# Performance work log

Measured on AMD Instinct MI355X. Metric: run time of the kernel, lower is better.

## Reference

```python
import jax, jax.numpy as jnp
import numpy as np

# Fixed architecture constants from the source
B, T, D, V, L, H = 4096, 128, 64, 65, 3, 8
HD = D // H  # head_size = 8
DF = 4 * D   # 256


def _layernorm(x, g, b, eps=1e-5):
    mu = jnp.mean(x, axis=-1, keepdims=True)
    var = jnp.mean(jnp.square(x - mu), axis=-1, keepdims=True)
    return (x - mu) * jax.lax.rsqrt(var + eps) * g + b


def setup_inputs() -> dict:
    key = jax.random.key(0)
    ks = iter(jax.random.split(key, 64))
    s = 0.02
    n = lambda shape: jax.random.normal(next(ks), shape, dtype=jnp.float32) * s
    inp = {
        "tok_emb": n((V, D)),
        "pos_emb": n((T, D)),
        # per-block params stacked on leading layer dim L=3
        "ln1_g": jnp.ones((L, D), jnp.float32), "ln1_b": jnp.zeros((L, D), jnp.float32),
        "wq": n((L, D, D)), "wk": n((L, D, D)), "wv": n((L, D, D)),
        "wo": n((L, D, D)), "bo": jnp.zeros((L, D), jnp.float32),
        "ln2_g": jnp.ones((L, D), jnp.float32), "ln2_b": jnp.zeros((L, D), jnp.float32),
        "w1": n((L, D, DF)), "b1": jnp.zeros((L, DF), jnp.float32),
        "w2": n((L, DF, D)), "b2": jnp.zeros((L, D), jnp.float32),
        "lnf_g": jnp.ones((D,), jnp.float32), "lnf_b": jnp.zeros((D,), jnp.float32),
        "lm_w": n((D, V)), "lm_b": jnp.zeros((V,), jnp.float32),
        "idx": jax.random.randint(next(ks), (B, T), 0, V),
        "targets": jax.random.randint(next(ks), (B, T), 0, V),
    }
    return inp


def _forward(tok_emb, pos_emb, ln1_g, ln1_b, wq, wk, wv, wo, bo,
             ln2_g, ln2_b, w1, b1, w2, b2, lnf_g, lnf_b, lm_w, lm_b,
             idx, targets):
    b, t = idx.shape
    x = tok_emb[idx] + pos_emb[:t]  # [B,T,D]
    mask = jnp.tril(jnp.ones((t, t), bool))
    scale = 1.0 / np.sqrt(HD)
    for l in range(L):  # 3 structurally identical blocks (dropout = identity at eval)
        xn = _layernorm(x, ln1_g[l], ln1_b[l])
        # 8 per-head projections fused into one [D,D] matmul (concat along out dim)
        q = (xn @ wq[l]).reshape(b, t, H, HD)
        k = (xn @ wk[l]).reshape(b, t, H, HD)
        v = (xn @ wv[l]).reshape(b, t, H, HD)
        scores = jnp.einsum('bqhd,bkhd->bhqk', q, k) * scale
        scores = jnp.where(mask, scores, -jnp.inf)
        probs = jax.nn.softmax(scores, axis=-1)
        attn = jnp.einsum('bhqk,bkhd->bqhd', probs, v).reshape(b, t, D)
        x = x + attn @ wo[l] + bo[l]
        xn = _layernorm(x, ln2_g[l], ln2_b[l])
        x = x + jax.nn.relu(xn @ w1[l] + b1[l]) @ w2[l] + b2[l]
    x = _layernorm(x, lnf_g, lnf_b)
    logits = (x @ lm_w + lm_b).reshape(b * t, V)
    logp = jax.nn.log_softmax(logits, axis=-1)
    loss = -jnp.mean(jnp.take_along_axis(logp, targets.reshape(b * t, 1), axis=1))
    return logits, loss


def reference(tok_emb, pos_emb, ln1_g, ln1_b, wq, wk, wv, wo, bo,
              ln2_g, ln2_b, w1, b1, w2, b2, lnf_g, lnf_b, lm_w, lm_b,
              idx, targets):
    return _forward(tok_emb, pos_emb, ln1_g, ln1_b, wq, wk, wv, wo, bo,
                    ln2_g, ln2_b, w1, b1, w2, b2, lnf_g, lnf_b, lm_w, lm_b,
                    idx, targets)
```

## Files before the change

### kernel.cpp

```cpp
#include <hip/hip_runtime.h>
#include <hip/hip_bf16.h>

#define NB  4096
#define NT  128
#define ND  64
#define NV  65
#define NL  3
#define NH  8
#define NDF 256
#define NBT (NB*NT)

#define OFF_TOK   0
#define OFF_POS   4160
#define OFF_LN1G  12352
#define OFF_LN1B  12544
#define OFF_WQ    12736
#define OFF_WK    25024
#define OFF_WV    37312
#define OFF_WO    49600
#define OFF_BO    61888
#define OFF_LN2G  62080
#define OFF_LN2B  62272
#define OFF_W1    62464
#define OFF_B1    111616
#define OFF_W2    112384
#define OFF_B2    161536
#define OFF_LNFG  161728
#define OFF_LNFB  161792
#define OFF_LMW   161856
#define OFF_LMB   166016
#define CVT_TOTAL 166081
#define OFF_LOSS  166144
#define OFF_FLAG  166145

#define PKF       166148
#define PK_ELEMS  147456
#define NEED_WS   ((size_t)(PKF + PK_ELEMS) * 4)

typedef short s8v  __attribute__((ext_vector_type(8)));
typedef float f4v  __attribute__((ext_vector_type(4)));

struct CvtArgs { const void* p[19]; };

__device__ __forceinline__ unsigned short f2bf(float x) {
    unsigned int u = __float_as_uint(x);
    u = (u + 0x7fffu + ((u >> 16) & 1u)) >> 16;
    return (unsigned short)u;
}
__device__ __forceinline__ float bf2f(unsigned short h) {
    return __uint_as_float(((unsigned int)h) << 16);
}
__device__ __forceinline__ f4v mfma16(s8v a, s8v b, f4v c) {
    return __builtin_amdgcn_mfma_f32_16x16x32_bf16(a, b, c, 0, 0, 0);
}

__global__ void diag_fill(float* __restrict__ out, int n, float val) {
    int i = blockIdx.x * 256 + threadIdx.x;
    if (i < n) out[i] = val;
}

__global__ void detect_float(const unsigned short* __restrict__ tok,
                             int* __restrict__ flags) {
    int bad = 0;
    for (int i = threadIdx.x; i < 4096; i += 256) {
        float v = __uint_as_float(((unsigned int)tok[i]) << 16);
        if (!(fabsf(v) < 1000.f)) bad = 1;
    }
    if (bad) atomicOr(flags, 1);
}

__global__ void detect_int(const int* __restrict__ idx32,
                           int* __restrict__ flags) {
    int proven = 0;
    #pragma unroll
    for (int j = 0; j < 8; j++) {
        int slot = 2 * (threadIdx.x * 8 + j) + 1;
        if (idx32[slot] != 0) proven = 1;
    }
    if (proven) atomicOr(flags, 4);
}

__global__ void cvt_params(CvtArgs a, float* __restrict__ W,
                           const int* __restrict__ flags) {
    int tid = blockIdx.x * 256 + threadIdx.x;
    if (tid >= CVT_TOTAL) return;
    const int offs[20] = {0,4160,12352,12544,12736,25024,37312,49600,61888,
                          62080,62272,62464,111616,112384,161536,161728,
                          161792,161856,166016,166081};
    int s = 0;
    #pragma unroll
    for (int k = 1; k < 19; k++) s += (tid >= offs[k]);
    int local = tid - offs[s];
    if (*flags & 1) {
        W[tid] = ((const float*)a.p[s])[local];
    } else {
        unsigned int v = ((const unsigned short*)a.p[s])[local];
        W[tid] = __uint_as_float(v << 16);
    }
}

__global__ void pack_weights(const float* __restrict__ W,
                             unsigned short* __restrict__ pkw) {
    int p = blockIdx.x * 256 + threadIdx.x;
    if (p >= PK_ELEMS) return;
    int srcoff, K, N, perlay, local, ktbits;
    if (p < 49152) {
        int grp = p / 12288; local = p % 12288;
        srcoff = (grp == 0) ? OFF_WQ : (grp == 1) ? OFF_WK
               : (grp == 2) ? OFF_WV : OFF_WO;
        K = 64; N = 64; perlay = 4096; ktbits = 1;
    } else if (p < 98304) {
        local = p - 49152; srcoff = OFF_W1; K = 64; N = 256;
        perlay = 16384; ktbits = 1;
    } else {
        local = p - 98304; srcoff = OFF_W2; K = 256; N = 64;
        perlay = 16384; ktbits = 3;
    }
    int lay = local / perlay, rem = local % perlay;
    int t = rem >> 9, le = rem & 511, l = le >> 3, e = le & 7;
    int kt = t & ((1 << ktbits) - 1), nt = t >> ktbits;
    int row = kt * 32 + (l >> 4) * 8 + e;
    int col = nt * 16 + (l & 15);
    float v = W[srcoff + lay * K * N + row * N + col];
    unsigned short hi = f2bf(v);
    pkw[p] = hi;
    pkw[PK_ELEMS + p] = f2bf(v - bf2f(hi));
}

__global__ void mfma_probe(int* __restrict__ flags) {
    int l = threadIdx.x;
    s8v av, bv;
    int i = l & 15;
    #pragma unroll
    for (int e = 0; e < 8; e++) {
        int k = (l >> 4) * 8 + e;
        av[e] = (short)f2bf((float)(((i * 5 + k * 3) & 7) - 3));
        bv[e] = (short)f2bf((float)(((k * 7 + i * 11) & 7) - 4));
    }
    f4v c = {0.f, 0.f, 0.f, 0.f};
    c = mfma16(av, bv, c);
    int bad = 0;
    #pragma unroll
    for (int reg = 0; reg < 4; reg++) {
        int row = (l >> 4) * 4 + reg, col = l & 15;
        float exp = 0.f;
        for (int k = 0; k < 32; k++)
            exp += (float)(((row * 5 + k * 3) & 7) - 3) *
                   (float)(((k * 7 + col * 11) & 7) - 4);
        if (c[reg] != exp) bad = 1;
    }
    if (bad) atomicOr(flags, 8);
}

__device__ __forceinline__ void unpack8(uint4 u, float* f) {
    f[0] = __uint_as_float(u.x << 16); f[1] = __uint_as_float(u.x & 0xffff0000u);
    f[2] = __uint_as_float(u.y << 16); f[3] = __uint_as_float(u.y & 0xffff0000u);
    f[4] = __uint_as_float(u.z << 16); f[5] = __uint_as_float(u.z & 0xffff0000u);
    f[6] = __uint_as_float(u.w << 16); f[7] = __uint_as_float(u.w & 0xffff0000u);
}

__device__ __forceinline__ void ln_rm(const float (*src)[68], float (*dst)[68],
                                      const float* __restrict__ g,
                                      const float* __restrict__ bb, int tid) {
    int r = tid >> 3, q = tid & 7;
    int c0 = q * 8;
    float s = 0.f, s2 = 0.f;
    #pragma unroll
    for (int c = 0; c < 8; c++) { float v = src[r][c0 + c]; s += v; s2 += v * v; }
    s += __shfl_xor(s, 1);  s2 += __shfl_xor(s2, 1);
    s += __shfl_xor(s, 2);  s2 += __shfl_xor(s2, 2);
    s += __shfl_xor(s, 4);  s2 += __shfl_xor(s2, 4);
    float mu   = s  * (1.f / 64.f);
    float var  = s2 * (1.f / 64.f) - mu * mu;
    float rstd = rsqrtf(var + 1e-5f);
    #pragma unroll
    for (int c = 0; c < 8; c++) {
        int cc = c0 + c;
        dst[r][cc] = (src[r][cc] - mu) * rstd * g[cc] + bb[cc];
    }
}

__device__ __forceinline__ void ln_frag(const float (*src)[68],
        unsigned short* __restrict__ dhi, unsigned short* __restrict__ dlo,
        const float* __restrict__ g, const float* __restrict__ bb, int tid) {
    int r = tid >> 3, q = tid & 7, c0 = q * 8;
    float s = 0.f, s2 = 0.f;
    #pragma unroll
    for (int c = 0; c < 8; c++) { float v = src[r][c0 + c]; s += v; s2 += v * v; }
    s += __shfl_xor(s, 1);  s2 += __shfl_xor(s2, 1);
    s += __shfl_xor(s, 2);  s2 += __shfl_xor(s2, 2);
    s += __shfl_xor(s, 4);  s2 += __shfl_xor(s2, 4);
    float mu   = s  * (1.f / 64.f);
    float var  = s2 * (1.f / 64.f) - mu * mu;
    float rstd = rsqrtf(var + 1e-5f);
    unsigned uh[4], ul[4];
    #pragma unroll
    for (int c2 = 0; c2 < 4; c2++) {
        float y0 = (src[r][c0 + c2*2    ] - mu) * rstd * g[c0 + c2*2    ] + bb[c0 + c2*2    ];
        float y1 = (src[r][c0 + c2*2 + 1] - mu) * rstd * g[c0 + c2*2 + 1] + bb[c0 + c2*2 + 1];
        unsigned short h0 = f2bf(y0), h1 = f2bf(y1);
        uh[c2] = (unsigned)h0 | ((unsigned)h1 << 16);
        ul[c2] = (unsigned)f2bf(y0 - bf2f(h0)) | ((unsigned)f2bf(y1 - bf2f(h1)) << 16);
    }
    int di = (((r >> 4) * 2 + (q >> 2)) * 64 + (q & 3) * 16 + (r & 15)) * 8;
    *(uint4*)(dhi + di) = make_uint4(uh[0], uh[1], uh[2], uh[3]);
    *(uint4*)(dlo + di) = make_uint4(ul[0], ul[1], ul[2], ul[3]);
}

__device__ __forceinline__ void fma16(const float* xr, const float* wr, float& a) {
    float4 x0 = *(const float4*)(xr);
    float4 x1 = *(const float4*)(xr + 4);
    float4 x2 = *(const float4*)(xr + 8);
    float4 x3 = *(const float4*)(xr + 12);
    a = fmaf(x0.x, wr[0],  a); a = fmaf(x0.y, wr[1],  a);
    a = fmaf(x0.z, wr[2],  a); a = fmaf(x0.w, wr[3],  a);
    a = fmaf(x1.x, wr[4],  a); a = fmaf(x1.y, wr[5],  a);
    a = fmaf(x1.z, wr[6],  a); a = fmaf(x1.w, wr[7],  a);
    a = fmaf(x2.x, wr[8],  a); a = fmaf(x2.y, wr[9],  a);
    a = fmaf(x2.z, wr[10], a); a = fmaf(x2.w, wr[11], a);
    a = fmaf(x3.x, wr[12], a); a = fmaf(x3.y, wr[13], a);
    a = fmaf(x3.z, wr[14], a); a = fmaf(x3.w, wr[15], a);
}

__device__ void ln_scalar(const float* x, float* o,
                          const float* g, const float* bb) {
    float mu = 0.f;
    for (int i = 0; i < ND; i++) mu += x[i];
    mu *= (1.f / 64.f);
    float var = 0.f;
    for (int i = 0; i < ND; i++) { float d = x[i] - mu; var += d * d; }
    var *= (1.f / 64.f);
    float rstd = rsqrtf(var + 1e-5f);
    for (int i = 0; i < ND; i++) o[i] = (x[i] - mu) * rstd * g[i] + bb[i];
}

__global__ __launch_bounds__(1024, 4) void gpt_fwd(
    const float* __restrict__ W, const unsigned short* __restrict__ pkw,
    int usepk, const void* __restrict__ idxp, const void* __restrict__ tgtp,
    float* __restrict__ out, float* __restrict__ loss_acc,
    const int* __restrict__ flags)
{
    __shared__ alignas(16) float xs[NT][68];
    __shared__ alignas(16) unsigned char regB[34816];
    __shared__ alignas(16) unsigned char uni[65536];
    __shared__ alignas(16) unsigned short zblk[8];
    __shared__ float wsum[16];

    float (*xnR)[68] = (float (*)[68])regB;
    unsigned short* xah = (unsigned short*)regB;
    unsigned short* xal = (unsigned short*)(regB + 16384);
    unsigned short* q_lds = (unsigned short*)uni;
    unsigned short* k_lds = (unsigned short*)(uni + 16384);
    unsigned short* vb    = (unsigned short*)(uni + 32768);
    unsigned short (*qs)[72] = (unsigned short (*)[72])(uni);
    unsigned short (*ks)[72] = (unsigned short (*)[72])(uni + 18432);
    unsigned short (*vs)[72] = (unsigned short (*)[72])(uni + 36864);
    unsigned short* ha = (unsigned short*)uni;
    unsigned short* hl = (unsigned short*)(uni + 32768);
    float (*hch)[264] = (float (*)[264])uni;

    const int tid  = threadIdx.x;
    const int lane = tid & 63;
    const int w    = tid >> 6;
    const int b    = blockIdx.x;
    const int fl   = *flags;
    const bool i64 = !(fl & 4);
    const bool use_mfma = usepk && !(fl & 8);
    const int*       idx32 = (const int*)idxp;
    const long long* idx64 = (const long long*)idxp;
    const int*       tgt32 = (const int*)tgtp;
    const long long* tgt64 = (const long long*)tgtp;

    if (tid < 8) zblk[tid] = 0;

    for (int e = tid * 4; e < NT * ND; e += 4096) {
        int r = e >> 6, c = e & 63;
        int n = b * NT + r;
        int tok = i64 ? (int)idx64[n] : idx32[n];
        float4 te = *(const float4*)&W[OFF_TOK + tok * ND + c];
        float4 pe = *(const float4*)&W[OFF_POS + r * ND + c];
        float4 xv;
        xv.x = te.x + pe.x; xv.y = te.y + pe.y;
        xv.z = te.z + pe.z; xv.w = te.w + pe.w;
        *(float4*)&xs[r][c] = xv;
    }
    __syncthreads();

    if (use_mfma) {
        for (int lay = 0; lay < NL; lay++) {
            ln_frag(xs, xah, xal, W + OFF_LN1G + lay * 64, W + OFF_LN1B + lay * 64, tid);
            __syncthreads();

            {
                const unsigned short* pbase = pkw + lay * 4096;
                #pragma unroll 1
                for (int i = 0; i < 6; i++) {
                    int ft = w * 6 + i;
                    int mat = ft >> 5, mt = (ft >> 2) & 7, nt = ft & 3;
                    const unsigned short* pb = pbase + mat * 12288 + nt * 1024 + lane * 8;
                    f4v acc = {0.f, 0.f, 0.f, 0.f};
                    #pragma unroll
                    for (int kt = 0; kt < 2; kt++) {
                        s8v ah = *(const s8v*)(xah + ((mt * 2 + kt) * 64 + lane) * 8);
                        s8v al = *(const s8v*)(xal + ((mt * 2 + kt) * 64 + lane) * 8);
                        s8v bh = *(const s8v*)(pb + kt * 512);
                        s8v bl = *(const s8v*)(pb + PK_ELEMS + kt * 512);
                        acc = mfma16(ah, bh, acc);
                        acc = mfma16(ah, bl, acc);
                        acc = mfma16(al, bh, acc);
                    }
                    int row0 = mt * 16 + (lane >> 4) * 4;
                    int fullcol = nt * 16 + (lane & 15);
                    int head = fullcol >> 3, dim = fullcol & 7;
                    if (mat == 0) {
                        #pragma unroll
                        for (int i2 = 0; i2 < 4; i2++)
                            q_lds[(head * 128 + row0 + i2) * 8 + dim] =
                                f2bf(acc[i2] * 0.35355339059327373f);
                    } else if (mat == 1) {
                        #pragma unroll
                        for (int i2 = 0; i2 < 4; i2++)
                            k_lds[(head * 128 + row0 + i2) * 8 + dim] = f2bf(acc[i2]);
                    } else {
                        #pragma unroll
                        for (int i2 = 0; i2 < 4; i2++) {
                            int key = row0 + i2;
                            vb[((((head * 4) + (key >> 5)) * 4 + ((key >> 3) & 3)) * 8
                                + dim) * 8 + (key & 7)] = f2bf(acc[i2]);
                        }
                    }
                }
            }
            __syncthreads();

            {
                unsigned short* pscr = (unsigned short*)(uni + 49152) + w * 512;
                const int cl = lane & 15, g = lane >> 4;
                #pragma unroll 1
                for (int ti = 0; ti < 4; ti++) {
                    int t = w + ti * 16;
                    int mt = t >> 3, head = t & 7;
                    const unsigned short* qsrc = (lane < 16)
                        ? q_lds + (head * 128 + mt * 16 + cl) * 8 : zblk;
                    s8v qa = *(const s8v*)qsrc;
                    f4v sv[8];
                    #pragma unroll
                    for (int nt = 0; nt < 8; nt++) {
                        sv[nt] = (f4v){0.f, 0.f, 0.f, 0.f};
                        if (nt <= mt) {
                            const unsigned short* ksrc = (lane < 16)
                                ? k_lds + (head * 128 + nt * 16 + cl) * 8 : zblk;
                            s8v kb = *(const s8v*)ksrc;
                            sv[nt] = mfma16(qa, kb, sv[nt]);
                            if (nt == mt) {
                                #pragma unroll
                                for (int i2 = 0; i2 < 4; i2++)
                                    sv[nt][i2] = (cl <= g * 4 + i2) ? sv[nt][i2] : -1e30f;
                            }
                        }
                    }
                    float mx[4] = {-1e30f, -1e30f, -1e30f, -1e30f};
                    #pragma unroll
                    for (int nt = 0; nt < 8; nt++)
                        if (nt <= mt) {
                            #pragma unroll
                            for (int i2 = 0; i2 < 4; i2++)
                                mx[i2] = fmaxf(mx[i2], sv[nt][i2]);
                        }
                    #pragma unroll
                    for (int i2 = 0; i2 < 4; i2++) {
                        mx[i2] = fmaxf(mx[i2], __shfl_xor(mx[i2], 1));
                        mx[i2] = fmaxf(mx[i2], __shfl_xor(mx[i2], 2));
                        mx[i2] = fmaxf(mx[i2], __shfl_xor(mx[i2], 4));
                        mx[i2] = fmaxf(mx[i2], __shfl_xor(mx[i2], 8));
                    }
                    float sm[4] = {0.f, 0.f, 0.f, 0.f};
                    #pragma unroll
                    for (int nt = 0; nt < 8; nt++)
                        if (nt <= mt) {
                            #pragma unroll
                            for (int i2 = 0; i2 < 4; i2++) {
                                float p = __expf(sv[nt][i2] - mx[i2]);
                                sv[nt][i2] = p;
                                sm[i2] += p;
                            }
                        }
                    #pragma unroll
                    for (int i2 = 0; i2 < 4; i2++) {
                        sm[i2] += __shfl_xor(sm[i2], 1);
                        sm[i2] += __shfl_xor(sm[i2], 2);
                        sm[i2] += __shfl_xor(sm[i2], 4);
                        sm[i2] += __shfl_xor(sm[i2], 8);
                    }
                    float inv[4];
                    #pragma unroll
                    for (int i2 = 0; i2 < 4; i2++) inv[i2] = 1.f / sm[i2];
                    f4v o = {0.f, 0.f, 0.f, 0.f};
                    #pragma unroll
                    for (int kt = 0; kt < 4; kt++) {
                        if (kt <= (mt >> 1)) {
                            #pragma unroll
                            for (int s2 = 0; s2 < 2; s2++) {
                                int nt = kt * 2 + s2;
                                #pragma unroll
                                for (int i2 = 0; i2 < 4; i2++) {
                                    float pv = (nt <= mt) ? sv[nt][i2] * inv[i2] : 0.f;
                                    pscr[(g * 4 + i2) * 32 + s2 * 16 + cl] = f2bf(pv);
                                }
                            }
                            s8v pa = *(const s8v*)(pscr + cl * 32 + g * 8);
                            const unsigned short* vsrc = (cl < 8)
                                ? vb + ((((head * 4) + kt) * 4 + g) * 8 + cl) * 8 : zblk;
                            s8v vf = *(const s8v*)vsrc;
                            o = mfma16(pa, vf, o);
                        }
                    }
                    if (cl < 8) {
                        #pragma unroll
                        for (int i2 = 0; i2 < 4; i2++) {
                            int r = mt * 16 + g * 4 + i2;
                            float y = o[i2];
                            unsigned short h = f2bf(y);
                            int di = (((r >> 4) * 2 + (head >> 2)) * 64
                                      + (head & 3) * 16 + (r & 15)) * 8 + cl;
                            xah[di] = h;
                            xal[di] = f2bf(y - bf2f(h));
                        }
                    }
                }
            }
            __syncthreads();

            {
                const unsigned short* pbase = pkw + 36864 + lay * 4096;
                const float* bo = W + OFF_BO + lay * 64;
                #pragma unroll 1
                for (int i = 0; i < 2; i++) {
                    int ft = w * 2 + i;
                    int mt = ft >> 2, nt = ft & 3;
                    const unsigned short* pb = pbase + nt * 1024 + lane * 8;
                    f4v acc = {0.f, 0.f, 0.f, 0.f};
                    #pragma unroll
                    for (int kt = 0; kt < 2; kt++) {
                        s8v ah = *(const s8v*)(xah + ((mt * 2 + kt) * 64 + lane) * 8);
                        s8v al = *(const s8v*)(xal + ((mt * 2 + kt) * 64 + lane) * 8);
                        s8v bh = *(const s8v*)(pb + kt * 512);
                        s8v bl = *(const s8v*)(pb + PK_ELEMS + kt * 512);
                        acc = mfma16(ah, bh, acc);
                        acc = mfma16(ah, bl, acc);
                        acc = mfma16(al, bh, acc);
                    }
                    int row0 = mt * 16 + (lane >> 4) * 4, col = nt * 16 + (lane & 15);
                    float bias = bo[col];
                    xs[row0    ][col] += acc[0] + bias;
                    xs[row0 + 1][col] += acc[1] + bias;
                    xs[row0 + 2][col] += acc[2] + bias;
                    xs[row0 + 3][col] += acc[3] + bias;
                }
            }
            __syncthreads();

            ln_frag(xs, xah, xal, W + OFF_LN2G + lay * 64, W + OFF_LN2B + lay * 64, tid);
            __syncthreads();

            for (int hh = 0; hh < 2; hh++) {
                {
                    const float* b1 = W + OFF_B1 + lay * 256;
                    #pragma unroll 1
                    for (int i = 0; i < 4; i++) {
                        int ft = w * 4 + i;
                        int mtl = ft >> 4, nt = ft & 15;
                        int mt = hh * 4 + mtl;
                        const unsigned short* pb = pkw + 49152 + lay * 16384 + nt * 1024 + lane * 8;
                        f4v acc = {0.f, 0.f, 0.f, 0.f};
                        #pragma unroll
                        for (int kt = 0; kt < 2; kt++) {
                            s8v ah = *(const s8v*)(xah + ((mt * 2 + kt) * 64 + lane) * 8);
                            s8v al = *(const s8v*)(xal + ((mt * 2 + kt) * 64 + lane) * 8);
                            s8v bh = *(const s8v*)(pb + kt * 512);
                            s8v bl = *(const s8v*)(pb + PK_ELEMS + kt * 512);
                            acc = mfma16(ah, bh, acc);
                            acc = mfma16(ah, bl, acc);
                            acc = mfma16(al, bh, acc);
                        }
                        int col = nt * 16 + (lane & 15);
                        float bias = b1[col];
                        int kt2 = col >> 5, q2 = (col >> 3) & 3, e2 = col & 7;
                        #pragma unroll
                        for (int i2 = 0; i2 < 4; i2++) {
                            int lr = mtl * 16 + (lane >> 4) * 4 + i2;
                            float hvv = fmaxf(acc[i2] + bias, 0.f);
                            int di = ((mtl * 8 + kt2) * 64 + q2 * 16 + (lr & 15)) * 8 + e2;
                            unsigned short hi = f2bf(hvv);
                            ha[di] = hi;
                            hl[di] = f2bf(hvv - bf2f(hi));
                        }
                    }
                }
                __syncthreads();
                {
                    const float* b2 = W + OFF_B2 + lay * 64;
                    int mtl = w >> 2, nt = w & 3;
                    const unsigned short* pb = pkw + 98304 + lay * 16384 + nt * 4096 + lane * 8;
                    f4v acc = {0.f, 0.f, 0.f, 0.f};
                    #pragma unroll 2
                    for (int kt = 0; kt < 8; kt++) {
                        s8v ah = *(const s8v*)(ha + ((mtl * 8 + kt) * 64 + lane) * 8);
                        s8v al = *(const s8v*)(hl + ((mtl * 8 + kt) * 64 + lane) * 8);
                        s8v bh = *(const s8v*)(pb + kt * 512);
                        s8v bl = *(const s8v*)(pb + PK_ELEMS + kt * 512);
                        acc = mfma16(ah, bh, acc);
                        acc = mfma16(ah, bl, acc);
                        acc = mfma16(al, bh, acc);
                    }
                    int row0 = hh * 64 + mtl * 16 + (lane >> 4) * 4, col = nt * 16 + (lane & 15);
                    float bias = b2[col];
                    xs[row0    ][col] += acc[0] + bias;
                    xs[row0 + 1][col] += acc[1] + bias;
                    xs[row0 + 2][col] += acc[2] + bias;
                    xs[row0 + 3][col] += acc[3] + bias;
                }
                __syncthreads();
            }
        }
        ln_rm(xs, xnR, W + OFF_LNFG, W + OFF_LNFB, tid);
        __syncthreads();
    } else {
        for (int lay = 0; lay < NL; lay++) {
            ln_rm(xs, xnR, W + OFF_LN1G + lay * 64, W + OFF_LN1B + lay * 64, tid);
            __syncthreads();
            {
                #pragma unroll 1
                for (int mmat = 0; mmat < 3; mmat++) {
                    const float* wm = W + (mmat == 0 ? OFF_WQ : (mmat == 1 ? OFF_WK : OFF_WV))
                                        + lay * ND * ND;
                    unsigned short (*dstp)[72] = (mmat == 0) ? qs : ((mmat == 1) ? ks : vs);
                    float acc[8];
                    #pragma unroll
                    for (int rr = 0; rr < 8; rr++) acc[rr] = 0.f;
                    #pragma unroll 1
                    for (int ih = 0; ih < 4; ih++) {
                        float wr[16];
                        #pragma unroll
                        for (int i = 0; i < 16; i++) wr[i] = wm[(ih * 16 + i) * ND + lane];
                        #pragma unroll
                        for (int rr = 0; rr < 8; rr++)
                            fma16(&xnR[w * 8 + rr][ih * 16], wr, acc[rr]);
                    }
                    #pragma unroll
                    for (int rr = 0; rr < 8; rr++)
                        dstp[w * 8 + rr][lane] = f2bf(acc[rr]);
                }
            }
            __syncthreads();
            {
                const int head = w & 7, hh = w >> 3;
                const int h8 = head * 8;
                const int r  = lane + hh * 64;
                const float scale = 0.35355339059327373f;
                float qv[8];
                uint4 qq = *(const uint4*)&qs[r][h8];
                unpack8(qq, qv);
                #pragma unroll
                for (int d = 0; d < 8; d++) qv[d] *= scale;
                float m = -1e30f, lsum = 0.f;
                float o[8] = {0, 0, 0, 0, 0, 0, 0, 0};
                for (int base = 0; base <= r; base += 8) {
                    float sc[8];
                    #pragma unroll
                    for (int t = 0; t < 8; t++) {
                        int kk = base + t; kk = kk > 127 ? 127 : kk;
                        uint4 kr = *(const uint4*)&ks[kk][h8];
                        float kf[8]; unpack8(kr, kf);
                        float s = 0.f;
                        #pragma unroll
                        for (int d = 0; d < 8; d++) s = fmaf(qv[d], kf[d], s);
                        sc[t] = (base + t <= r) ? s : -1e30f;
                    }
                    float cm = fmaxf(fmaxf(fmaxf(sc[0], sc[1]), fmaxf(sc[2], sc[3])),
                                     fmaxf(fmaxf(sc[4], sc[5]), fmaxf(sc[6], sc[7])));
                    float nm  = fmaxf(m, cm);
                    float fac = __expf(m - nm);
                    lsum *= fac;
                    #pragma unroll
                    for (int d = 0; d < 8; d++) o[d] *= fac;
                    #pragma unroll
                    for (int t = 0; t < 8; t++) {
                        float p = __expf(sc[t] - nm);
                        int kk = base + t; kk = kk > 127 ? 127 : kk;
                        uint4 vr = *(const uint4*)&vs[kk][h8];
                        float vf[8]; unpack8(vr, vf);
                        lsum += p;
                        #pragma unroll
                        for (int d = 0; d < 8; d++) o[d] = fmaf(p, vf[d], o[d]);
                    }
                    m = nm;
                }
                float inv = 1.f / lsum;
                #pragma unroll
                for (int d = 0; d < 8; d++) xnR[r][h8 + d] = o[d] * inv;
            }
            __syncthreads();
            {
                const float* wo = W + OFF_WO + lay * ND * ND;
                float acc[8];
                #pragma unroll
                for (int rr = 0; rr < 8; rr++) acc[rr] = W[OFF_BO + lay * ND + lane];
                #pragma unroll 1
                for (int ih = 0; ih < 4; ih++) {
                    float wr[16];
                    #pragma unroll
                    for (int i = 0; i < 16; i++) wr[i] = wo[(ih * 16 + i) * ND + lane];
                    #pragma unroll
                    for (int rr = 0; rr < 8; rr++)
                        fma16(&xnR[w * 8 + rr][ih * 16], wr, acc[rr]);
                }
                #pragma unroll
                for (int rr = 0; rr < 8; rr++)
                    xs[w * 8 + rr][lane] += acc[rr];
            }
            __syncthreads();
            ln_rm(xs, xnR, W + OFF_LN2G + lay * 64, W + OFF_LN2B + lay * 64, tid);
            __syncthreads();
            {
                const float* w1 = W + OFF_W1 + lay * ND * NDF;
                const float* w2 = W + OFF_W2 + lay * NDF * ND;
                const float* b1 = W + OFF_B1 + lay * NDF;
                const float* b2 = W + OFF_B2 + lay * ND;
                for (int ch = 0; ch < 4; ch++) {
                    int rbase = ch * 32;
                    {
                        int lr = tid >> 5;
                        int j0 = (tid & 31) * 8;
                        int r  = rbase + lr;
                        float4 ba  = *(const float4*)(b1 + j0);
                        float4 bb4 = *(const float4*)(b1 + j0 + 4);
                        float a0 = ba.x,  a1 = ba.y,  a2 = ba.z,  a3 = ba.w;
                        float a4 = bb4.x, a5 = bb4.y, a6 = bb4.z, a7 = bb4.w;
                        #pragma unroll 4
                        for (int i4 = 0; i4 < ND; i4 += 4) {
                            float4 xv = *(const float4*)&xnR[r][i4];
                            #pragma unroll
                            for (int s = 0; s < 4; s++) {
                                float xvs = (s == 0) ? xv.x : (s == 1) ? xv.y
                                          : (s == 2) ? xv.z : xv.w;
                                float4 wa = *(const float4*)(w1 + (i4 + s) * NDF + j0);
                                float4 wb = *(const float4*)(w1 + (i4 + s) * NDF + j0 + 4);
                                a0 = fmaf(xvs, wa.x, a0); a1 = fmaf(xvs, wa.y, a1);
                                a2 = fmaf(xvs, wa.z, a2); a3 = fmaf(xvs, wa.w, a3);
                                a4 = fmaf(xvs, wb.x, a4); a5 = fmaf(xvs, wb.y, a5);
                                a6 = fmaf(xvs, wb.z, a6); a7 = fmaf(xvs, wb.w, a7);
                            }
                        }
                        float4 h0, h1;
                        h0.x = fmaxf(a0, 0.f); h0.y = fmaxf(a1, 0.f);
                        h0.z = fmaxf(a2, 0.f); h0.w = fmaxf(a3, 0.f);
                        h1.x = fmaxf(a4, 0.f); h1.y = fmaxf(a5, 0.f);
                        h1.z = fmaxf(a6, 0.f); h1.w = fmaxf(a7, 0.f);
                        *(float4*)&hch[lr][j0]     = h0;
                        *(float4*)&hch[lr][j0 + 4] = h1;
                    }
                    __syncthreads();
                    {
                        int lr = tid >> 5;
                        int i0 = (tid & 31) * 2;
                        int r  = rbase + lr;
                        float a0 = 0.f, a1 = 0.f;
                        #pragma unroll 4
                        for (int j4 = 0; j4 < NDF; j4 += 4) {
                            float4 hv = *(const float4*)&hch[lr][j4];
                            #pragma unroll
                            for (int s = 0; s < 4; s++) {
                                float hvs = (s == 0) ? hv.x : (s == 1) ? hv.y
                                          : (s == 2) ? hv.z : hv.w;
                                float2 w2v = *(const float2*)(w2 + (j4 + s) * ND + i0);
                                a0 = fmaf(hvs, w2v.x, a0); a1 = fmaf(hvs, w2v.y, a1);
                            }
                        }
                        float2 bb2 = *(const float2*)(b2 + i0);
                        xs[r][i0]     += a0 + bb2.x;
                        xs[r][i0 + 1] += a1 + bb2.y;
                    }
                    __syncthreads();
                }
            }
        }
        ln_rm(xs, xnR, W + OFF_LNFG, W + OFF_LNFB, tid);
        __syncthreads();
    }

    {
        const float* lmw = W + OFF_LMW;
        float wacc = 0.f;
        for (int rr = 0; rr < 8; rr++) {
            int r = w * 8 + rr;
            float lg  = W[OFF_LMB + lane];
            float lg2 = W[OFF_LMB + 64];
            #pragma unroll 8
            for (int i = 0; i < ND; i++) {
                float xv = xnR[r][i];
                lg  = fmaf(xv, lmw[i * NV + lane], lg);
                lg2 = fmaf(xv, lmw[i * NV + 64],  lg2);
            }
            float M = lg;
            #pragma unroll
            for (int off = 32; off; off >>= 1) M = fmaxf(M, __shfl_xor(M, off));
            M = fmaxf(M, lg2);
            float ssum = __expf(lg - M);
            #pragma unroll
            for (int off = 32; off; off >>= 1) ssum += __shfl_xor(ssum, off);
            ssum += __expf(lg2 - M);
            float lse = M + logf(ssum);
            int row = b * NT + r;
            int tg  = i64 ? (int)tgt64[row] : tgt32[row];
            float lt = (tg < 64) ? __shfl(lg, tg) : lg2;
            wacc += lt - lse;
            out[row * NV + lane] = lg;
            if (lane == 0) out[row * NV + 64] = lg2;
        }
        if (lane == 0) wsum[w] = wacc;
        __syncthreads();
        if (tid == 0) {
            float t = 0.f;
            #pragma unroll
            for (int wv = 0; wv < 16; wv++) t += wsum[wv];
            atomicAdd(loss_acc, t);
        }
    }
    __syncthreads();

    if (b == 0 && tid == 0) {
        float x0[ND], xn0[ND], v0[ND], h0[NDF];
        int tok0 = i64 ? (int)idx64[0] : idx32[0];
        for (int c = 0; c < ND; c++)
            x0[c] = W[OFF_TOK + tok0 * ND + c] + W[OFF_POS + c];
        for (int l = 0; l < NL; l++) {
            ln_scalar(x0, xn0, W + OFF_LN1G + l * ND, W + OFF_LN1B + l * ND);
            for (int c = 0; c < ND; c++) {
                float a = 0.f;
                for (int i = 0; i < ND; i++)
                    a += xn0[i] * W[OFF_WV + l * ND * ND + i * ND + c];
                v0[c] = a;
            }
            for (int c = 0; c < ND; c++) {
                float a = W[OFF_BO + l * ND + c];
                for (int i = 0; i < ND; i++)
                    a += v0[i] * W[OFF_WO + l * ND * ND + i * ND + c];
                x0[c] += a;
            }
            ln_scalar(x0, xn0, W + OFF_LN2G + l * ND, W + OFF_LN2B + l * ND);
            for (int j = 0; j < NDF; j++) {
                float a = W[OFF_B1 + l * NDF + j];
                for (int i = 0; i < ND; i++)
                    a += xn0[i] * W[OFF_W1 + l * ND * NDF + i * NDF + j];
                h0[j] = fmaxf(a, 0.f);
            }
            for (int c = 0; c < ND; c++) {
                float a = W[OFF_B2 + l * ND + c];
                for (int j = 0; j < NDF; j++)
                    a += h0[j] * W[OFF_W2 + l * NDF * ND + j * ND + c];
                x0[c] += a;
            }
        }
        ln_scalar(x0, xn0, W + OFF_LNFG, W + OFF_LNFB);
        bool bad = false;
        for (int v = 0; v < NV; v++) {
            float lg = W[OFF_LMB + v];
            for (int i = 0; i < ND; i++)
                lg += xn0[i] * W[OFF_LMW + i * NV + v];
            if (!(fabsf(out[v] - lg) <= 0.05f)) bad = true;
        }
        if (bad) out[0] = 100.0f;
    }
}

__global__ void finalize_loss(const float* __restrict__ acc,
                              float* __restrict__ out) {
    out[NBT * NV] = -acc[0] * (1.f / (float)NBT);
}

extern "C" void kernel_launch(void* const* d_in, const int* in_sizes, int n_in,
                              void* d_out, int out_size, void* d_ws, size_t ws_size,
                              hipStream_t stream)
{
    static const int want[21] = {4160, 8192, 192, 192, 12288, 12288, 12288,
                                 12288, 192, 192, 192, 49152, 768, 49152, 192,
                                 64, 64, 4160, 65, 524288, 524288};
    int diag = 0;
    if (n_in != 21) diag = 3;
    else for (int i = 0; i < 21; i++) if (in_sizes[i] != want[i]) { diag = 3; break; }
    if (!diag && out_size != NBT * NV + 1) diag = 4;
    if (!diag && ws_size < (size_t)(OFF_FLAG + 1) * 4) diag = 5;
    if (diag) {
        diag_fill<<<(out_size + 255) / 256, 256, 0, stream>>>(
            (float*)d_out, out_size, (float)diag);
        return;
    }

    float* W = (float*)d_ws;
    float* loss_acc = W + OFF_LOSS;
    int*   flags    = (int*)(W + OFF_FLAG);
    hipMemsetAsync(W + OFF_LOSS, 0, 2 * sizeof(float), stream);

    detect_float<<<1, 256, 0, stream>>>((const unsigned short*)d_in[0], flags);
    detect_int  <<<1, 256, 0, stream>>>((const int*)d_in[19], flags);
    mfma_probe  <<<1, 64,  0, stream>>>(flags);

    CvtArgs a;
    for (int i = 0; i < 19; i++) a.p[i] = d_in[i];
    cvt_params<<<(CVT_TOTAL + 255) / 256, 256, 0, stream>>>(a, W, flags);

    int usepk = (ws_size >= NEED_WS) ? 1 : 0;
    unsigned short* pkw = (unsigned short*)(W + PKF);
    if (usepk)
        pack_weights<<<(PK_ELEMS + 255) / 256, 256, 0, stream>>>(W, pkw);

    gpt_fwd<<<NB, 1024, 0, stream>>>(W, pkw, usepk, d_in[19], d_in[20],
                                     (float*)d_out, loss_acc, flags);
    finalize_loss<<<1, 1, 0, stream>>>(loss_acc, (float*)d_out);
}
```

Measured before the change: 2.466 ms.

## Shrink LDS footprint, split QKV by head halves, use online-softmax MFMA attention

The main kernel now processes attention in two halves of four heads each, which reduces shared memory from roughly 100KB to about 50KB and raises the launch-bounds occupancy hint from 4 to 8. The activation low-order bf16 split is dropped, so projections use two MFMAs per k-step instead of three. Attention becomes a flash-style online softmax that passes P through shuffles rather than an LDS scratch buffer. The lm_head weights are added to the packed buffer, and the old non-MFMA path moves into a separate gpt_fwd_valu kernel that is also launched. Dropping the low part of the activations lowers precision, and the extra launch may cost time if it does not exit early.

```diff
diff --git a/kernel.cpp b/kernel.cpp
--- a/kernel.cpp
+++ b/kernel.cpp
@@ -34,7 +34,8 @@
 #define OFF_FLAG  166145
 
 #define PKF       166148
-#define PK_ELEMS  147456
+#define PK_ELEMS  151552
+#define PKLO      151552
 #define NEED_WS   ((size_t)(PKF + PK_ELEMS) * 4)
 
 typedef short s8v  __attribute__((ext_vector_type(8)));
@@ -112,9 +113,12 @@
     } else if (p < 98304) {
         local = p - 49152; srcoff = OFF_W1; K = 64; N = 256;
         perlay = 16384; ktbits = 1;
-    } else {
+    } else if (p < 147456) {
         local = p - 98304; srcoff = OFF_W2; K = 256; N = 64;
         perlay = 16384; ktbits = 3;
+    } else {
+        local = p - 147456; srcoff = OFF_LMW; K = 64; N = 65;
+        perlay = 4096; ktbits = 1;
     }
     int lay = local / perlay, rem = local % perlay;
     int t = rem >> 9, le = rem & 511, l = le >> 3, e = le & 7;
@@ -124,7 +128,7 @@
     float v = W[srcoff + lay * K * N + row * N + col];
     unsigned short hi = f2bf(v);
     pkw[p] = hi;
-    pkw[PK_ELEMS + p] = f2bf(v - bf2f(hi));
+    pkw[PKLO + p] = f2bf(v - bf2f(hi));
 }
 
 __global__ void mfma_probe(int* __restrict__ flags) {
@@ -180,8 +184,8 @@
     }
 }
 
-__device__ __forceinline__ void ln_frag(const float (*src)[68],
-        unsigned short* __restrict__ dhi, unsigned short* __restrict__ dlo,
+__device__ __forceinline__ void ln_frag_hi(const float (*src)[68],
+        unsigned short* __restrict__ dhi,
         const float* __restrict__ g, const float* __restrict__ bb, int tid) {
     int r = tid >> 3, q = tid & 7, c0 = q * 8;
     float s = 0.f, s2 = 0.f;
@@ -193,18 +197,15 @@
     float mu   = s  * (1.f / 64.f);
     float var  = s2 * (1.f / 64.f) - mu * mu;
     float rstd = rsqrtf(var + 1e-5f);
-    unsigned uh[4], ul[4];
+    unsigned uh[4];
     #pragma unroll
     for (int c2 = 0; c2 < 4; c2++) {
         float y0 = (src[r][c0 + c2*2    ] - mu) * rstd * g[c0 + c2*2    ] + bb[c0 + c2*2    ];
         float y1 = (src[r][c0 + c2*2 + 1] - mu) * rstd * g[c0 + c2*2 + 1] + bb[c0 + c2*2 + 1];
-        unsigned short h0 = f2bf(y0), h1 = f2bf(y1);
-        uh[c2] = (unsigned)h0 | ((unsigned)h1 << 16);
-        ul[c2] = (unsigned)f2bf(y0 - bf2f(h0)) | ((unsigned)f2bf(y1 - bf2f(h1)) << 16);
+        uh[c2] = (unsigned)f2bf(y0) | ((unsigned)f2bf(y1) << 16);
     }
     int di = (((r >> 4) * 2 + (q >> 2)) * 64 + (q & 3) * 16 + (r & 15)) * 8;
     *(uint4*)(dhi + di) = make_uint4(uh[0], uh[1], uh[2], uh[3]);
-    *(uint4*)(dlo + di) = make_uint4(ul[0], ul[1], ul[2], ul[3]);
 }
 
 __device__ __forceinline__ void fma16(const float* xr, const float* wr, float& a) {
@@ -234,38 +235,49 @@
     for (int i = 0; i < ND; i++) o[i] = (x[i] - mu) * rstd * g[i] + bb[i];
 }
 
-__global__ __launch_bounds__(1024, 4) void gpt_fwd(
+__device__ __forceinline__ void store_o(unsigned short* xah, int mt, int head,
+                                        int g, int cl, unsigned pk0, unsigned pk1) {
+    if (cl < 8) {
+        unsigned pk[2] = {pk0, pk1};
+        #pragma unroll
+        for (int i2 = 0; i2 < 4; i2++) {
+            int r = mt * 16 + g * 4 + i2;
+            int col = head * 8 + cl;
+            unsigned v = pk[i2 >> 1];
+            unsigned short hv = (unsigned short)((i2 & 1) ? (v >> 16) : (v & 0xffffu));
+            int di = (((r >> 4) * 2 + (col >> 5)) * 64 + ((col >> 3) & 3) * 16
+                      + (r & 15)) * 8 + (col & 7);
+            xah[di] = hv;
+        }
+    }
+}
+
+__global__ __launch_bounds__(1024, 8) void gpt_fwd(
     const float* __restrict__ W, const unsigned short* __restrict__ pkw,
     int usepk, const void* __restrict__ idxp, const void* __restrict__ tgtp,
     float* __restrict__ out, float* __restrict__ loss_acc,
     const int* __restrict__ flags)
 {
     __shared__ alignas(16) float xs[NT][68];
-    __shared__ alignas(16) unsigned char regB[34816];
-    __shared__ alignas(16) unsigned char uni[65536];
+    __shared__ alignas(16) unsigned short xah[8192];
+    __shared__ alignas(16) unsigned short uni[12288];
     __shared__ alignas(16) unsigned short zblk[8];
-    __shared__ float wsum[16];
-
-    float (*xnR)[68] = (float (*)[68])regB;
-    unsigned short* xah = (unsigned short*)regB;
-    unsigned short* xal = (unsigned short*)(regB + 16384);
-    unsigned short* q_lds = (unsigned short*)uni;
-    unsigned short* k_lds = (unsigned short*)(uni + 16384);
-    unsigned short* vb    = (unsigned short*)(uni + 32768);
-    unsigned short (*qs)[72] = (unsigned short (*)[72])(uni);
-    unsigned short (*ks)[72] = (unsigned short (*)[72])(uni + 18432);
-    unsigned short (*vs)[72] = (unsigned short (*)[72])(uni + 36864);
-    unsigned short* ha = (unsigned short*)uni;
-    unsigned short* hl = (unsigned short*)(uni + 32768);
-    float (*hch)[264] = (float (*)[264])uni;
+    __shared__ float wsum[8];
+
+    unsigned short* q_l = uni;
+    unsigned short* k_l = uni + 4096;
+    unsigned short* vb  = uni + 8192;
+    unsigned short* ha  = uni;
 
     const int tid  = threadIdx.x;
     const int lane = tid & 63;
     const int w    = tid >> 6;
+    const int cl   = lane & 15;
+    const int g    = lane >> 4;
     const int b    = blockIdx.x;
     const int fl   = *flags;
+    if (!usepk || (fl & 8)) return;
     const bool i64 = !(fl & 4);
-    const bool use_mfma = usepk && !(fl & 8);
     const int*       idx32 = (const int*)idxp;
     const long long* idx64 = (const long long*)idxp;
     const int*       tgt32 = (const int*)tgtp;
@@ -286,47 +298,52 @@
     }
     __syncthreads();
 
-    if (use_mfma) {
-        for (int lay = 0; lay < NL; lay++) {
-            ln_frag(xs, xah, xal, W + OFF_LN1G + lay * 64, W + OFF_LN1B + lay * 64, tid);
-            __syncthreads();
-
+    for (int lay = 0; lay < NL; lay++) {
+        ln_frag_hi(xs, xah, W + OFF_LN1G + lay * 64, W + OFF_LN1B + lay * 64, tid);
+        __syncthreads();
+
+        unsigned ostash[2][2];
+        const int headl = w & 3;
+
+        #pragma unroll 1
+        for (int hf = 0; hf < 2; hf++) {
             {
                 const unsigned short* pbase = pkw + lay * 4096;
                 #pragma unroll 1
-                for (int i = 0; i < 6; i++) {
-                    int ft = w * 6 + i;
-                    int mat = ft >> 5, mt = (ft >> 2) & 7, nt = ft & 3;
-                    const unsigned short* pb = pbase + mat * 12288 + nt * 1024 + lane * 8;
+                for (int i = 0; i < 3; i++) {
+                    int ft = w * 3 + i;
+                    int mat = ft >> 4;
+                    int mt  = (ft >> 1) & 7;
+                    int ntg = hf * 2 + (ft & 1);
+                    const unsigned short* pb = pbase + mat * 12288 + ntg * 1024 + lane * 8;
                     f4v acc = {0.f, 0.f, 0.f, 0.f};
                     #pragma unroll
                     for (int kt = 0; kt < 2; kt++) {
                         s8v ah = *(const s8v*)(xah + ((mt * 2 + kt) * 64 + lane) * 8);
-                        s8v al = *(const s8v*)(xal + ((mt * 2 + kt) * 64 + lane) * 8);
                         s8v bh = *(const s8v*)(pb + kt * 512);
-                        s8v bl = *(const s8v*)(pb + PK_ELEMS + kt * 512);
+                        s8v bl = *(const s8v*)(pb + PKLO + kt * 512);
                         acc = mfma16(ah, bh, acc);
                         acc = mfma16(ah, bl, acc);
-                        acc = mfma16(al, bh, acc);
                     }
-                    int row0 = mt * 16 + (lane >> 4) * 4;
-                    int fullcol = nt * 16 + (lane & 15);
-                    int head = fullcol >> 3, dim = fullcol & 7;
+                    int row0 = mt * 16 + g * 4;
+                    int fullcol = ntg * 16 + cl;
+                    int hl2 = (fullcol >> 3) & 3;
+                    int dim = fullcol & 7;
                     if (mat == 0) {
                         #pragma unroll
                         for (int i2 = 0; i2 < 4; i2++)
-                            q_lds[(head * 128 + row0 + i2) * 8 + dim] =
+                            q_l[(hl2 * 128 + row0 + i2) * 8 + dim] =
                                 f2bf(acc[i2] * 0.35355339059327373f);
                     } else if (mat == 1) {
                         #pragma unroll
                         for (int i2 = 0; i2 < 4; i2++)
-                            k_lds[(head * 128 + row0 + i2) * 8 + dim] = f2bf(acc[i2]);
+                            k_l[(hl2 * 128 + row0 + i2) * 8 + dim] = f2bf(acc[i2]);
                     } else {
                         #pragma unroll
                         for (int i2 = 0; i2 < 4; i2++) {
                             int key = row0 + i2;
-                            vb[((((head * 4) + (key >> 5)) * 4 + ((key >> 3) & 3)) * 8
-                                + dim) * 8 + (key & 7)] = f2bf(acc[i2]);
+                            vb[((hl2 * 4 + (key >> 5)) * 4 + ((key >> 3) & 3)) * 64
+                               + dim * 8 + (key & 7)] = f2bf(acc[i2]);
                         }
                     }
                 }
@@ -334,171 +351,169 @@
             __syncthreads();
 
             {
-                unsigned short* pscr = (unsigned short*)(uni + 49152) + w * 512;
-                const int cl = lane & 15, g = lane >> 4;
                 #pragma unroll 1
-                for (int ti = 0; ti < 4; ti++) {
-                    int t = w + ti * 16;
-                    int mt = t >> 3, head = t & 7;
+                for (int ti = 0; ti < 2; ti++) {
+                    int mt = (w >> 2) + ti * 4;
                     const unsigned short* qsrc = (lane < 16)
-                        ? q_lds + (head * 128 + mt * 16 + cl) * 8 : zblk;
-                    s8v qa = *(const s8v*)qsrc;
-                    f4v sv[8];
-                    #pragma unroll
-                    for (int nt = 0; nt < 8; nt++) {
-                        sv[nt] = (f4v){0.f, 0.f, 0.f, 0.f};
-                        if (nt <= mt) {
+                        ? q_l + (headl * 128 + mt * 16 + cl) * 8 : zblk;
+                    s8v qb = *(const s8v*)qsrc;
+                    float m = -1e30f, lsum = 0.f;
+                    f4v o = {0.f, 0.f, 0.f, 0.f};
+                    const int ktmax = mt >> 1;
+                    #pragma unroll 1
+                    for (int kt = 0; kt <= ktmax; kt++) {
+                        f4v p0, p1;
+                        {
                             const unsigned short* ksrc = (lane < 16)
-                                ? k_lds + (head * 128 + nt * 16 + cl) * 8 : zblk;
+                                ? k_l + (headl * 128 + (kt * 2) * 16 + cl) * 8 : zblk;
                             s8v kb = *(const s8v*)ksrc;
-                            sv[nt] = mfma16(qa, kb, sv[nt]);
-                            if (nt == mt) {
+                            f4v s0 = {0.f, 0.f, 0.f, 0.f};
+                            s0 = mfma16(kb, qb, s0);
+                            if (kt * 2 == mt) {
                                 #pragma unroll
                                 for (int i2 = 0; i2 < 4; i2++)
-                                    sv[nt][i2] = (cl <= g * 4 + i2) ? sv[nt][i2] : -1e30f;
+                                    s0[i2] = (g * 4 + i2 <= cl) ? s0[i2] : -1e30f;
                             }
+                            p0 = s0;
                         }
-                    }
-                    float mx[4] = {-1e30f, -1e30f, -1e30f, -1e30f};
-                    #pragma unroll
-                    for (int nt = 0; nt < 8; nt++)
-                        if (nt <= mt) {
-                            #pragma unroll
-                            for (int i2 = 0; i2 < 4; i2++)
-                                mx[i2] = fmaxf(mx[i2], sv[nt][i2]);
+                        if (kt * 2 + 1 <= mt) {
+                            const unsigned short* ksrc = (lane < 16)
+                                ? k_l + (headl * 128 + (kt * 2 + 1) * 16 + cl) * 8 : zblk;
+                            s8v kb = *(const s8v*)ksrc;
+                            f4v s1 = {0.f, 0.f, 0.f, 0.f};
+                            s1 = mfma16(kb, qb, s1);
+                            if (kt * 2 + 1 == mt) {
+                                #pragma unroll
+                                for (int i2 = 0; i2 < 4; i2++)
+                                    s1[i2] = (g * 4 + i2 <= cl) ? s1[i2] : -1e30f;
+                            }
+                            p1 = s1;
+                        } else {
+                            p1 = (f4v){-1e30f, -1e30f, -1e30f, -1e30f};
                         }
-                    #pragma unroll
-                    for (int i2 = 0; i2 < 4; i2++) {
-                        mx[i2] = fmaxf(mx[i2], __shfl_xor(mx[i2], 1));
-                        mx[i2] = fmaxf(mx[i2], __shfl_xor(mx[i2], 2));
-                        mx[i2] = fmaxf(mx[i2], __shfl_xor(mx[i2], 4));
-                        mx[i2] = fmaxf(mx[i2], __shfl_xor(mx[i2], 8));
-                    }
-                    float sm[4] = {0.f, 0.f, 0.f, 0.f};
-                    #pragma unroll
-                    for (int nt = 0; nt < 8; nt++)
-                        if (nt <= mt) {
-                            #pragma unroll
-                            for (int i2 = 0; i2 < 4; i2++) {
-                                float p = __expf(sv[nt][i2] - mx[i2]);
-                                sv[nt][i2] = p;
-                                sm[i2] += p;
-                            }
-                        }
-                    #pragma unroll
-                    for (int i2 = 0; i2 < 4; i2++) {
-                        sm[i2] += __shfl_xor(sm[i2], 1);
-                        sm[i2] += __shfl_xor(sm[i2], 2);
-                        sm[i2] += __shfl_xor(sm[i2], 4);
-                        sm[i2] += __shfl_xor(sm[i2], 8);
-                    }
-                    float inv[4];
-                    #pragma unroll
-                    for (int i2 = 0; i2 < 4; i2++) inv[i2] = 1.f / sm[i2];
-                    f4v o = {0.f, 0.f, 0.f, 0.f};
-                    #pragma unroll
-                    for (int kt = 0; kt < 4; kt++) {
-                        if (kt <= (mt >> 1)) {
-                            #pragma unroll
-                            for (int s2 = 0; s2 < 2; s2++) {
-                                int nt = kt * 2 + s2;
-                                #pragma unroll
-                                for (int i2 = 0; i2 < 4; i2++) {
-                                    float pv = (nt <= mt) ? sv[nt][i2] * inv[i2] : 0.f;
-                                    pscr[(g * 4 + i2) * 32 + s2 * 16 + cl] = f2bf(pv);
-                                }
-                            }
-                            s8v pa = *(const s8v*)(pscr + cl * 32 + g * 8);
-                            const unsigned short* vsrc = (cl < 8)
-                                ? vb + ((((head * 4) + kt) * 4 + g) * 8 + cl) * 8 : zblk;
-                            s8v vf = *(const s8v*)vsrc;
-                            o = mfma16(pa, vf, o);
-                        }
-                    }
-                    if (cl < 8) {
+                        float bm = fmaxf(fmaxf(fmaxf(p0[0], p0[1]), fmaxf(p0[2], p0[3])),
+                                         fmaxf(fmaxf(p1[0], p1[1]), fmaxf(p1[2], p1[3])));
+                        bm = fmaxf(bm, __shfl_xor(bm, 16));
+                        bm = fmaxf(bm, __shfl_xor(bm, 32));
+                        float nm  = fmaxf(m, bm);
+                        float fac = __expf(m - nm);
+                        float ps = 0.f;
                         #pragma unroll
                         for (int i2 = 0; i2 < 4; i2++) {
-                            int r = mt * 16 + g * 4 + i2;
-                            float y = o[i2];
-                            unsigned short h = f2bf(y);
-                            int di = (((r >> 4) * 2 + (head >> 2)) * 64
-                                      + (head & 3) * 16 + (r & 15)) * 8 + cl;
-                            xah[di] = h;
-                            xal[di] = f2bf(y - bf2f(h));
+                            p0[i2] = __expf(p0[i2] - nm); ps += p0[i2];
+                            p1[i2] = __expf(p1[i2] - nm); ps += p1[i2];
                         }
+                        ps += __shfl_xor(ps, 16);
+                        ps += __shfl_xor(ps, 32);
+                        lsum = lsum * fac + ps;
+                        #pragma unroll
+                        for (int i2 = 0; i2 < 4; i2++)
+                            o[i2] *= __shfl(fac, g * 4 + i2);
+                        float pe[8];
+                        #pragma unroll
+                        for (int e = 0; e < 8; e++) {
+                            int src = ((g & 1) * 2 + (e >> 2)) * 16 + cl;
+                            float a0 = __shfl(p0[e & 3], src);
+                            float a1 = __shfl(p1[e & 3], src);
+                            pe[e] = (g >> 1) ? a1 : a0;
+                        }
+                        union { unsigned u[4]; s8v v; } pu;
+                        #pragma unroll
+                        for (int j = 0; j < 4; j++)
+                            pu.u[j] = (unsigned)f2bf(pe[2 * j]) |
+                                      ((unsigned)f2bf(pe[2 * j + 1]) << 16);
+                        s8v vf = *(const s8v*)(vb + ((headl * 4 + kt) * 4 + g) * 64
+                                               + (cl & 7) * 8);
+                        o = mfma16(pu.v, vf, o);
+                        m = nm;
                     }
+                    float inv = 1.f / lsum;
+                    float invt[4];
+                    #pragma unroll
+                    for (int i2 = 0; i2 < 4; i2++) invt[i2] = __shfl(inv, g * 4 + i2);
+                    unsigned pk0 = (unsigned)f2bf(o[0] * invt[0]) |
+                                   ((unsigned)f2bf(o[1] * invt[1]) << 16);
+                    unsigned pk1 = (unsigned)f2bf(o[2] * invt[2]) |
+                                   ((unsigned)f2bf(o[3] * invt[3]) << 16);
+                    if (hf == 0) {
+                        ostash[ti][0] = pk0; ostash[ti][1] = pk1;
+                    } else {
+                        store_o(xah, mt, 4 + headl, g, cl, pk0, pk1);
+                    }
+                }
+                if (hf == 1) {
+                    #pragma unroll
+                    for (int ti = 0; ti < 2; ti++) {
+                        int mt = (w >> 2) + ti * 4;
+                        store_o(xah, mt, headl, g, cl, ostash[ti][0], ostash[ti][1]);
+                    }
                 }
             }
             __syncthreads();
-
+        }
+
+        {
+            const unsigned short* pbase = pkw + 36864 + lay * 4096;
+            const float* bo = W + OFF_BO + lay * 64;
+            #pragma unroll 1
+            for (int i = 0; i < 2; i++) {
+                int ft = w * 2 + i;
+                int mt = ft >> 2, nt = ft & 3;
+                const unsigned short* pb = pbase + nt * 1024 + lane * 8;
+                f4v acc = {0.f, 0.f, 0.f, 0.f};
+                #pragma unroll
+                for (int kt = 0; kt < 2; kt++) {
+                    s8v ah = *(const s8v*)(xah + ((mt * 2 + kt) * 64 + lane) * 8);
+                    s8v bh = *(const s8v*)(pb + kt * 512);
+                    s8v bl = *(const s8v*)(pb + PKLO + kt * 512);
+                    acc = mfma16(ah, bh, acc);
+                    acc = mfma16(ah, bl, acc);
+                }
+                int row0 = mt * 16 + g * 4, col = nt * 16 + cl;
+                float bias = bo[col];
+                #pragma unroll
+                for (int i2 = 0; i2 < 4; i2++)
+                    xs[row0 + i2][col] += acc[i2] + bias;
+            }
+        }
+        __syncthreads();
+
+        ln_frag_hi(xs, xah, W + OFF_LN2G + lay * 64, W + OFF_LN2B + lay * 64, tid);
+        __syncthreads();
+
+        #pragma unroll 1
+        for (int ch = 0; ch < 4; ch++) {
             {
-                const unsigned short* pbase = pkw + 36864 + lay * 4096;
-                const float* bo = W + OFF_BO + lay * 64;
+                const float* b1 = W + OFF_B1 + lay * 256;
                 #pragma unroll 1
                 for (int i = 0; i < 2; i++) {
                     int ft = w * 2 + i;
-                    int mt = ft >> 2, nt = ft & 3;
-                    const unsigned short* pb = pbase + nt * 1024 + lane * 8;
+                    int mtl = ft >> 4, nt = ft & 15;
+                    int mtg = ch * 2 + mtl;
+                    const unsigned short* pb = pkw + 49152 + lay * 16384 + nt * 1024 + lane * 8;
                     f4v acc = {0.f, 0.f, 0.f, 0.f};
                     #pragma unroll
                     for (int kt = 0; kt < 2; kt++) {
-                        s8v ah = *(const s8v*)(xah + ((mt * 2 + kt) * 64 + lane) * 8);
-                        s8v al = *(const s8v*)(xal + ((mt * 2 + kt) * 64 + lane) * 8);
+                        s8v ah = *(const s8v*)(xah + ((mtg * 2 + kt) * 64 + lane) * 8);
                         s8v bh = *(const s8v*)(pb + kt * 512);
-                        s8v bl = *(const s8v*)(pb + PK_ELEMS + kt * 512);
+                        s8v bl = *(const s8v*)(pb + PKLO + kt * 512);
                         acc = mfma16(ah, bh, acc);
                         acc = mfma16(ah, bl, acc);
-                        acc = mfma16(al, bh, acc);
                     }
-                    int row0 = mt * 16 + (lane >> 4) * 4, col = nt * 16 + (lane & 15);
-                    float bias = bo[col];
-                    xs[row0    ][col] += acc[0] + bias;
-                    xs[row0 + 1][col] += acc[1] + bias;
-                    xs[row0 + 2][col] += acc[2] + bias;
-                    xs[row0 + 3][col] += acc[3] + bias;
+                    int col = nt * 16 + cl;
+                    float bias = b1[col];
+                    int kt2 = col >> 5, q2 = (col >> 3) & 3, e2 = col & 7;
+                    #pragma unroll
+                    for (int i2 = 0; i2 < 4; i2++) {
+                        int lr = mtl * 16 + g * 4 + i2;
+                        float hv = fmaxf(acc[i2] + bias, 0.f);
+                        ha[((mtl * 8 + kt2) * 64 + q2 * 16 + (lr & 15)) * 8 + e2] = f2bf(hv);
+                    }
                 }
             }
             __syncthreads();
-
-            ln_frag(xs, xah, xal, W + OFF_LN2G + lay * 64, W + OFF_LN2B + lay * 64, tid);
-            __syncthreads();
-
-            for (int hh = 0; hh < 2; hh++) {
-                {
-                    const float* b1 = W + OFF_B1 + lay * 256;
-                    #pragma unroll 1
-                    for (int i = 0; i < 4; i++) {
-                        int ft = w * 4 + i;
-                        int mtl = ft >> 4, nt = ft & 15;
-                        int mt = hh * 4 + mtl;
-                        const unsigned short* pb = pkw + 49152 + lay * 16384 + nt * 1024 + lane * 8;
-                        f4v acc = {0.f, 0.f, 0.f, 0.f};
-                        #pragma unroll
-                        for (int kt = 0; kt < 2; kt++) {
-                            s8v ah = *(const s8v*)(xah + ((mt * 2 + kt) * 64 + lane) * 8);
-                            s8v al = *(const s8v*)(xal + ((mt * 2 + kt) * 64 + lane) * 8);
-                            s8v bh = *(const s8v*)(pb + kt * 512);
-                            s8v bl = *(const s8v*)(pb + PK_ELEMS + kt * 512);
-                            acc = mfma16(ah, bh, acc);
-                            acc = mfma16(ah, bl, acc);
-                            acc = mfma16(al, bh, acc);
-                        }
-                        int col = nt * 16 + (lane & 15);
-                        float bias = b1[col];
-                        int kt2 = col >> 5, q2 = (col >> 3) & 3, e2 = col & 7;
-                        #pragma unroll
-                        for (int i2 = 0; i2 < 4; i2++) {
-                            int lr = mtl * 16 + (lane >> 4) * 4 + i2;
-                            float hvv = fmaxf(acc[i2] + bias, 0.f);
-                            int di = ((mtl * 8 + kt2) * 64 + q2 * 16 + (lr & 15)) * 8 + e2;
-                            unsigned short hi = f2bf(hvv);
-                            ha[di] = hi;
-                            hl[di] = f2bf(hvv - bf2f(hi));
-                        }
-                    }
-                }
-                __syncthreads();
-                {
+            {
+                if (w < 8) {
                     const float* b2 = W + OFF_B2 + lay * 64;
                     int mtl = w >> 2, nt = w & 3;
                     const unsigned short* pb = pkw + 98304 + lay * 16384 + nt * 4096 + lane * 8;
@@ -506,226 +521,100 @@
                     #pragma unroll 2
                     for (int kt = 0; kt < 8; kt++) {
                         s8v ah = *(const s8v*)(ha + ((mtl * 8 + kt) * 64 + lane) * 8);
-                        s8v al = *(const s8v*)(hl + ((mtl * 8 + kt) * 64 + lane) * 8);
                         s8v bh = *(const s8v*)(pb + kt * 512);
-                        s8v bl = *(const s8v*)(pb + PK_ELEMS + kt * 512);
+                        s8v bl = *(const s8v*)(pb + PKLO + kt * 512);
                         acc = mfma16(ah, bh, acc);
                         acc = mfma16(ah, bl, acc);
-                        acc = mfma16(al, bh, acc);
                     }
-                    int row0 = hh * 64 + mtl * 16 + (lane >> 4) * 4, col = nt * 16 + (lane & 15);
+                    int row0 = ch * 32 + mtl * 16 + g * 4, col = nt * 16 + cl;
                     float bias = b2[col];
-                    xs[row0    ][col] += acc[0] + bias;
-                    xs[row0 + 1][col] += acc[1] + bias;
-                    xs[row0 + 2][col] += acc[2] + bias;
-                    xs[row0 + 3][col] += acc[3] + bias;
-                }
-                __syncthreads();
-            }
-        }
-        ln_rm(xs, xnR, W + OFF_LNFG, W + OFF_LNFB, tid);
-        __syncthreads();
-    } else {
-        for (int lay = 0; lay < NL; lay++) {
-            ln_rm(xs, xnR, W + OFF_LN1G + lay * 64, W + OFF_LN1B + lay * 64, tid);
+                    #pragma unroll
+                    for (int i2 = 0; i2 < 4; i2++)
+                        xs[row0 + i2][col] += acc[i2] + bias;
+                }
+            }
             __syncthreads();
-            {
-                #pragma unroll 1
-                for (int mmat = 0; mmat < 3; mmat++) {
-                    const float* wm = W + (mmat == 0 ? OFF_WQ : (mmat == 1 ? OFF_WK : OFF_WV))
-                                        + lay * ND * ND;
-                    unsigned short (*dstp)[72] = (mmat == 0) ? qs : ((mmat == 1) ? ks : vs);
-                    float acc[8];
-                    #pragma unroll
-                    for (int rr = 0; rr < 8; rr++) acc[rr] = 0.f;
-                    #pragma unroll 1
-                    for (int ih = 0; ih < 4; ih++) {
-                        float wr[16];
-                        #pragma unroll
-                        for (int i = 0; i < 16; i++) wr[i] = wm[(ih * 16 + i) * ND + lane];
-                        #pragma unroll
-                        for (int rr = 0; rr < 8; rr++)
-                            fma16(&xnR[w * 8 + rr][ih * 16], wr, acc[rr]);
-                    }
-                    #pragma unroll
-                    for (int rr = 0; rr < 8; rr++)
-                        dstp[w * 8 + rr][lane] = f2bf(acc[rr]);
-                }
-            }
-            __syncthreads();
-            {
-                const int head = w & 7, hh = w >> 3;
-                const int h8 = head * 8;
-                const int r  = lane + hh * 64;
-                const float scale = 0.35355339059327373f;
-                float qv[8];
-                uint4 qq = *(const uint4*)&qs[r][h8];
-                unpack8(qq, qv);
-                #pragma unroll
-                for (int d = 0; d < 8; d++) qv[d] *= scale;
-                float m = -1e30f, lsum = 0.f;
-                float o[8] = {0, 0, 0, 0, 0, 0, 0, 0};
-                for (int base = 0; base <= r; base += 8) {
-                    float sc[8];
-                    #pragma unroll
-                    for (int t = 0; t < 8; t++) {
-                        int kk = base + t; kk = kk > 127 ? 127 : kk;
-                        uint4 kr = *(const uint4*)&ks[kk][h8];
-                        float kf[8]; unpack8(kr, kf);
-                        float s = 0.f;
-                        #pragma unroll
-                        for (int d = 0; d < 8; d++) s = fmaf(qv[d], kf[d], s);
-                        sc[t] = (base + t <= r) ? s : -1e30f;
-                    }
-                    float cm = fmaxf(fmaxf(fmaxf(sc[0], sc[1]), fmaxf(sc[2], sc[3])),
-                                     fmaxf(fmaxf(sc[4], sc[5]), fmaxf(sc[6], sc[7])));
-                    float nm  = fmaxf(m, cm);
-                    float fac = __expf(m - nm);
-                    lsum *= fac;
-                    #pragma unroll
-                    for (int d = 0; d < 8; d++) o[d] *= fac;
-                    #pragma unroll
-                    for (int t = 0; t < 8; t++) {
-                        float p = __expf(sc[t] - nm);
-                        int kk = base + t; kk = kk > 127 ? 127 : kk;
-                        uint4 vr = *(const uint4*)&vs[kk][h8];
-                        float vf[8]; unpack8(vr, vf);
-                        lsum += p;
-                        #pragma unroll
-                        for (int d = 0; d < 8; d++) o[d] = fmaf(p, vf[d], o[d]);
-                    }
-                    m = nm;
-                }
-                float inv = 1.f / lsum;
-                #pragma unroll
-                for (int d = 0; d < 8; d++) xnR[r][h8 + d] = o[d] * inv;
-            }
-            __syncthreads();
-            {
-                const float* wo = W + OFF_WO + lay * ND * ND;
-                float acc[8];
-                #pragma unroll
-                for (int rr = 0; rr < 8; rr++) acc[rr] = W[OFF_BO + lay * ND + lane];
-                #pragma unroll 1
-                for (int ih = 0; ih < 4; ih++) {
-                    float wr[16];
-                    #pragma unroll
-                    for (int i = 0; i < 16; i++) wr[i] = wo[(ih * 16 + i) * ND + lane];
-                    #pragma unroll
-                    for (int rr = 0; rr < 8; rr++)
-                        fma16(&xnR[w * 8 + rr][ih * 16], wr, acc[rr]);
-                }
-                #pragma unroll
-                for (int rr = 0; rr < 8; rr++)
-                    xs[w * 8 + rr][lane] += acc[rr];
-            }
-            __syncthreads();
-            ln_rm(xs, xnR, W + OFF_LN2G + lay * 64, W + OFF_LN2B + lay * 64, tid);
-            __syncthreads();
-            {
-                const float* w1 = W + OFF_W1 + lay * ND * NDF;
-                const float* w2 = W + OFF_W2 + lay * NDF * ND;
-                const float* b1 = W + OFF_B1 + lay * NDF;
-                const float* b2 = W + OFF_B2 + lay * ND;
-                for (int ch = 0; ch < 4; ch++) {
-                    int rbase = ch * 32;
-                    {
-                        int lr = tid >> 5;
-                        int j0 = (tid & 31) * 8;
-                        int r  = rbase + lr;
-                        float4 ba  = *(const float4*)(b1 + j0);
-                        float4 bb4 = *(const float4*)(b1 + j0 + 4);
-                        float a0 = ba.x,  a1 = ba.y,  a2 = ba.z,  a3 = ba.w;
-                        float a4 = bb4.x, a5 = bb4.y, a6 = bb4.z, a7 = bb4.w;
-                        #pragma unroll 4
-                        for (int i4 = 0; i4 < ND; i4 += 4) {
-                            float4 xv = *(const float4*)&xnR[r][i4];
-                            #pragma unroll
-                            for (int s = 0; s < 4; s++) {
-                                float xvs = (s == 0) ? xv.x : (s == 1) ? xv.y
-                                          : (s == 2) ? xv.z : xv.w;
-                                float4 wa = *(const float4*)(w1 + (i4 + s) * NDF + j0);
-                                float4 wb = *(const float4*)(w1 + (i4 + s) * NDF + j0 + 4);
-                                a0 = fmaf(xvs, wa.x, a0); a1 = fmaf(xvs, wa.y, a1);
-                                a2 = fmaf(xvs, wa.z, a2); a3 = fmaf(xvs, wa.w, a3);
-                                a4 = fmaf(xvs, wb.x, a4); a5 = fmaf(xvs, wb.y, a5);
-                                a6 = fmaf(xvs, wb.z, a6); a7 = fmaf(xvs, wb.w, a7);
-                            }
-                        }
-                        float4 h0, h1;
-                        h0.x = fmaxf(a0, 0.f); h0.y = fmaxf(a1, 0.f);
-                        h0.z = fmaxf(a2, 0.f); h0.w = fmaxf(a3, 0.f);
-                        h1.x = fmaxf(a4, 0.f); h1.y = fmaxf(a5, 0.f);
-                        h1.z = fmaxf(a6, 0.f); h1.w = fmaxf(a7, 0.f);
-                        *(float4*)&hch[lr][j0]     = h0;
-                        *(float4*)&hch[lr][j0 + 4] = h1;
-                    }
-                    __syncthreads();
-                    {
-                        int lr = tid >> 5;
-                        int i0 = (tid & 31) * 2;
-                        int r  = rbase + lr;
-                        float a0 = 0.f, a1 = 0.f;
-                        #pragma unroll 4
-                        for (int j4 = 0; j4 < NDF; j4 += 4) {
-                            float4 hv = *(const float4*)&hch[lr][j4];
-                            #pragma unroll
-                            for (int s = 0; s < 4; s++) {
-                                float hvs = (s == 0) ? hv.x : (s == 1) ? hv.y
-                                          : (s == 2) ? hv.z : hv.w;
-                                float2 w2v = *(const float2*)(w2 + (j4 + s) * ND + i0);
-                                a0 = fmaf(hvs, w2v.x, a0); a1 = fmaf(hvs, w2v.y, a1);
-                            }
-                        }
-                        float2 bb2 = *(const float2*)(b2 + i0);
-                        xs[r][i0]     += a0 + bb2.x;
-                        xs[r][i0 + 1] += a1 + bb2.y;
-                    }
-                    __syncthreads();
-                }
-            }
-        }
-        ln_rm(xs, xnR, W + OFF_LNFG, W + OFF_LNFB, tid);
-        __syncthreads();
-    }
-
-    {
-        const float* lmw = W + OFF_LMW;
+        }
+    }
+
+    ln_frag_hi(xs, xah, W + OFF_LNFG, W + OFF_LNFB, tid);
+    __syncthreads();
+
+    if (w < 8) {
+        int mt = w;
+        const unsigned short* pb = pkw + 147456 + lane * 8;
+        f4v acc[4];
+        #pragma unroll
+        for (int nt = 0; nt < 4; nt++) {
+            f4v a = {0.f, 0.f, 0.f, 0.f};
+            #pragma unroll
+            for (int kt = 0; kt < 2; kt++) {
+                s8v ah = *(const s8v*)(xah + ((mt * 2 + kt) * 64 + lane) * 8);
+                s8v bh = *(const s8v*)(pb + nt * 1024 + kt * 512);
+                s8v bl = *(const s8v*)(pb + PKLO + nt * 1024 + kt * 512);
+                a = mfma16(ah, bh, a);
+                a = mfma16(ah, bl, a);
+            }
+            float bias = W[OFF_LMB + nt * 16 + cl];
+            #pragma unroll
+            for (int i2 = 0; i2 < 4; i2++) a[i2] += bias;
+            acc[nt] = a;
+        }
+        float l2 = 0.f;
+        #pragma unroll
+        for (int j = 0; j < 16; j++) {
+            int d = g * 16 + j;
+            int xi = ((mt * 2 + (d >> 5)) * 64 + ((d >> 3) & 3) * 16 + cl) * 8 + (d & 7);
+            l2 += bf2f(xah[xi]) * W[OFF_LMW + d * 65 + 64];
+        }
+        l2 += __shfl_xor(l2, 16);
+        l2 += __shfl_xor(l2, 32);
+        l2 += W[OFF_LMB + 64];
+        float l2t[4];
+        #pragma unroll
+        for (int i2 = 0; i2 < 4; i2++) l2t[i2] = __shfl(l2, g * 4 + i2);
+
         float wacc = 0.f;
-        for (int rr = 0; rr < 8; rr++) {
-            int r = w * 8 + rr;
-            float lg  = W[OFF_LMB + lane];
-            float lg2 = W[OFF_LMB + 64];
-            #pragma unroll 8
-            for (int i = 0; i < ND; i++) {
-                float xv = xnR[r][i];
-                lg  = fmaf(xv, lmw[i * NV + lane], lg);
-                lg2 = fmaf(xv, lmw[i * NV + 64],  lg2);
-            }
-            float M = lg;
-            #pragma unroll
-            for (int off = 32; off; off >>= 1) M = fmaxf(M, __shfl_xor(M, off));
-            M = fmaxf(M, lg2);
-            float ssum = __expf(lg - M);
-            #pragma unroll
-            for (int off = 32; off; off >>= 1) ssum += __shfl_xor(ssum, off);
-            ssum += __expf(lg2 - M);
-            float lse = M + logf(ssum);
+        #pragma unroll
+        for (int i2 = 0; i2 < 4; i2++) {
+            float M = fmaxf(fmaxf(acc[0][i2], acc[1][i2]), fmaxf(acc[2][i2], acc[3][i2]));
+            M = fmaxf(M, __shfl_xor(M, 1)); M = fmaxf(M, __shfl_xor(M, 2));
+            M = fmaxf(M, __shfl_xor(M, 4)); M = fmaxf(M, __shfl_xor(M, 8));
+            M = fmaxf(M, l2t[i2]);
+            float ss = __expf(acc[0][i2] - M) + __expf(acc[1][i2] - M)
+                     + __expf(acc[2][i2] - M) + __expf(acc[3][i2] - M);
+            ss += __shfl_xor(ss, 1); ss += __shfl_xor(ss, 2);
+            ss += __shfl_xor(ss, 4); ss += __shfl_xor(ss, 8);
+            ss += __expf(l2t[i2] - M);
+            float lse = M + logf(ss);
+            int r = mt * 16 + g * 4 + i2;
             int row = b * NT + r;
-            int tg  = i64 ? (int)tgt64[row] : tgt32[row];
-            float lt = (tg < 64) ? __shfl(lg, tg) : lg2;
-            wacc += lt - lse;
-            out[row * NV + lane] = lg;
-            if (lane == 0) out[row * NV + 64] = lg2;
-        }
+            int tg = i64 ? (int)tgt64[row] : tgt32[row];
+            float lt = 0.f;
+            #pragma unroll
+            for (int nt = 0; nt < 4; nt++)
+                if (nt * 16 + cl == tg) lt += acc[nt][i2];
+            wacc += lt;
+            if (cl == 0) {
+                if (tg == 64) wacc += l2t[i2];
+                wacc -= lse;
+                out[row * NV + 64] = l2t[i2];
+            }
+            #pragma unroll
+            for (int nt = 0; nt < 4; nt++)
+                out[row * NV + nt * 16 + cl] = acc[nt][i2];
+        }
+        wacc += __shfl_xor(wacc, 1);  wacc += __shfl_xor(wacc, 2);
+        wacc += __shfl_xor(wacc, 4);  wacc += __shfl_xor(wacc, 8);
+        wacc += __shfl_xor(wacc, 16); wacc += __shfl_xor(wacc, 32);
         if (lane == 0) wsum[w] = wacc;
-        __syncthreads();
-        if (tid == 0) {
-            float t = 0.f;
-            #pragma unroll
-            for (int wv = 0; wv < 16; wv++) t += wsum[wv];
-            atomicAdd(loss_acc, t);
-        }
+    }
+    __syncthreads();
+    if (tid == 0) {
+        float t = 0.f;
+        #pragma unroll
+        for (int wv = 0; wv < 8; wv++) t += wsum[wv];
+        atomicAdd(loss_acc, t);
     }
     __syncthreads();
 
@@ -771,6 +660,248 @@
             if (!(fabsf(out[v] - lg) <= 0.05f)) bad = true;
         }
         if (bad) out[0] = 100.0f;
+    }
+}
+
+__global__ __launch_bounds__(1024, 4) void gpt_fwd_valu(
+    const float* __restrict__ W, int usepk,
+    const void* __restrict__ idxp, const void* __restrict__ tgtp,
+    float* __restrict__ out, float* __restrict__ loss_acc,
+    const int* __restrict__ flags)
+{
+    const int fl = *flags;
+    if (usepk && !(fl & 8)) return;
+
+    __shared__ alignas(16) float xs[NT][68];
+    __shared__ alignas(16) float xn[NT][68];
+    __shared__ alignas(16) unsigned short qs[NT][72];
+    __shared__ alignas(16) unsigned short ks[NT][72];
+    __shared__ alignas(16) unsigned short vs[NT][72];
+    __shared__ alignas(16) float hch[32][264];
+    __shared__ float wsum[16];
+
+    const int tid  = threadIdx.x;
+    const int lane = tid & 63;
+    const int w    = tid >> 6;
+    const int b    = blockIdx.x;
+    const bool i64 = !(fl & 4);
+    const int*       idx32 = (const int*)idxp;
+    const long long* idx64 = (const long long*)idxp;
+    const int*       tgt32 = (const int*)tgtp;
+    const long long* tgt64 = (const long long*)tgtp;
+
+    for (int e = tid * 4; e < NT * ND; e += 4096) {
+        int r = e >> 6, c = e & 63;
+        int n = b * NT + r;
+        int tok = i64 ? (int)idx64[n] : idx32[n];
+        float4 te = *(const float4*)&W[OFF_TOK + tok * ND + c];
+        float4 pe = *(const float4*)&W[OFF_POS + r * ND + c];
+        float4 xv;
+        xv.x = te.x + pe.x; xv.y = te.y + pe.y;
+        xv.z = te.z + pe.z; xv.w = te.w + pe.w;
+        *(float4*)&xs[r][c] = xv;
+    }
+    __syncthreads();
+
+    for (int lay = 0; lay < NL; lay++) {
+        ln_rm(xs, xn, W + OFF_LN1G + lay * 64, W + OFF_LN1B + lay * 64, tid);
+        __syncthreads();
+        {
+            #pragma unroll 1
+            for (int mmat = 0; mmat < 3; mmat++) {
+                const float* wm = W + (mmat == 0 ? OFF_WQ : (mmat == 1 ? OFF_WK : OFF_WV))
+                                    + lay * ND * ND;
+                unsigned short (*dstp)[72] = (mmat == 0) ? qs : ((mmat == 1) ? ks : vs);
+                float acc[8];
+                #pragma unroll
+                for (int rr = 0; rr < 8; rr++) acc[rr] = 0.f;
+                #pragma unroll 1
+                for (int ih = 0; ih < 4; ih++) {
+                    float wr[16];
+                    #pragma unroll
+                    for (int i = 0; i < 16; i++) wr[i] = wm[(ih * 16 + i) * ND + lane];
+                    #pragma unroll
+                    for (int rr = 0; rr < 8; rr++)
+                        fma16(&xn[w * 8 + rr][ih * 16], wr, acc[rr]);
+                }
+                #pragma unroll
+                for (int rr = 0; rr < 8; rr++)
+                    dstp[w * 8 + rr][lane] = f2bf(acc[rr]);
+            }
+        }
+        __syncthreads();
+        {
+            const int head = w & 7, hh = w >> 3;
+            const int h8 = head * 8;
+            const int r  = lane + hh * 64;
+            const float scale = 0.35355339059327373f;
+            float qv[8];
+            uint4 qq = *(const uint4*)&qs[r][h8];
+            unpack8(qq, qv);
+            #pragma unroll
+            for (int d = 0; d < 8; d++) qv[d] *= scale;
+            float m = -1e30f, lsum = 0.f;
+            float o[8] = {0, 0, 0, 0, 0, 0, 0, 0};
+            for (int base = 0; base <= r; base += 8) {
+                float sc[8];
+                #pragma unroll
+                for (int t = 0; t < 8; t++) {
+                    int kk = base + t; kk = kk > 127 ? 127 : kk;
+                    uint4 kr = *(const uint4*)&ks[kk][h8];
+                    float kf[8]; unpack8(kr, kf);
+                    float s = 0.f;
+                    #pragma unroll
+                    for (int d = 0; d < 8; d++) s = fmaf(qv[d], kf[d], s);
+                    sc[t] = (base + t <= r) ? s : -1e30f;
+                }
+                float cm = fmaxf(fmaxf(fmaxf(sc[0], sc[1]), fmaxf(sc[2], sc[3])),
+                                 fmaxf(fmaxf(sc[4], sc[5]), fmaxf(sc[6], sc[7])));
+                float nm  = fmaxf(m, cm);
+                float fac = __expf(m - nm);
+                lsum *= fac;
+                #pragma unroll
+                for (int d = 0; d < 8; d++) o[d] *= fac;
+                #pragma unroll
+                for (int t = 0; t < 8; t++) {
+                    float p = __expf(sc[t] - nm);
+                    int kk = base + t; kk = kk > 127 ? 127 : kk;
+                    uint4 vr = *(const uint4*)&vs[kk][h8];
+                    float vf[8]; unpack8(vr, vf);
+                    lsum += p;
+                    #pragma unroll
+                    for (int d = 0; d < 8; d++) o[d] = fmaf(p, vf[d], o[d]);
+                }
+                m = nm;
+            }
+            float inv = 1.f / lsum;
+            #pragma unroll
+            for (int d = 0; d < 8; d++) xn[r][h8 + d] = o[d] * inv;
+        }
+        __syncthreads();
+        {
+            const float* wo = W + OFF_WO + lay * ND * ND;
+            float acc[8];
+            #pragma unroll
+            for (int rr = 0; rr < 8; rr++) acc[rr] = W[OFF_BO + lay * ND + lane];
+            #pragma unroll 1
+            for (int ih = 0; ih < 4; ih++) {
+                float wr[16];
+                #pragma unroll
+                for (int i = 0; i < 16; i++) wr[i] = wo[(ih * 16 + i) * ND + lane];
+                #pragma unroll
+                for (int rr = 0; rr < 8; rr++)
+                    fma16(&xn[w * 8 + rr][ih * 16], wr, acc[rr]);
+            }
+            #pragma unroll
+            for (int rr = 0; rr < 8; rr++)
+                xs[w * 8 + rr][lane] += acc[rr];
+        }
+        __syncthreads();
+        ln_rm(xs, xn, W + OFF_LN2G + lay * 64, W + OFF_LN2B + lay * 64, tid);
+        __syncthreads();
+        {
+            const float* w1 = W + OFF_W1 + lay * ND * NDF;
+            const float* w2 = W + OFF_W2 + lay * NDF * ND;
+            const float* b1 = W + OFF_B1 + lay * NDF;
+            const float* b2 = W + OFF_B2 + lay * ND;
+            for (int ch = 0; ch < 4; ch++) {
+                int rbase = ch * 32;
+                {
+                    int lr = tid >> 5;
+                    int j0 = (tid & 31) * 8;
+                    int r  = rbase + lr;
+                    float4 ba  = *(const float4*)(b1 + j0);
+                    float4 bb4 = *(const float4*)(b1 + j0 + 4);
+                    float a0 = ba.x,  a1 = ba.y,  a2 = ba.z,  a3 = ba.w;
+                    float a4 = bb4.x, a5 = bb4.y, a6 = bb4.z, a7 = bb4.w;
+                    #pragma unroll 4
+                    for (int i4 = 0; i4 < ND; i4 += 4) {
+                        float4 xv = *(const float4*)&xn[r][i4];
+                        #pragma unroll
+                        for (int s = 0; s < 4; s++) {
+                            float xvs = (s == 0) ? xv.x : (s == 1) ? xv.y
+                                      : (s == 2) ? xv.z : xv.w;
+                            float4 wa = *(const float4*)(w1 + (i4 + s) * NDF + j0);
+                            float4 wb = *(const float4*)(w1 + (i4 + s) * NDF + j0 + 4);
+                            a0 = fmaf(xvs, wa.x, a0); a1 = fmaf(xvs, wa.y, a1);
+                            a2 = fmaf(xvs, wa.z, a2); a3 = fmaf(xvs, wa.w, a3);
+                            a4 = fmaf(xvs, wb.x, a4); a5 = fmaf(xvs, wb.y, a5);
+                            a6 = fmaf(xvs, wb.z, a6); a7 = fmaf(xvs, wb.w, a7);
+                        }
+                    }
+                    float4 h0v, h1v;
+                    h0v.x = fmaxf(a0, 0.f); h0v.y = fmaxf(a1, 0.f);
+                    h0v.z = fmaxf(a2, 0.f); h0v.w = fmaxf(a3, 0.f);
+                    h1v.x = fmaxf(a4, 0.f); h1v.y = fmaxf(a5, 0.f);
+                    h1v.z = fmaxf(a6, 0.f); h1v.w = fmaxf(a7, 0.f);
+                    *(float4*)&hch[lr][j0]     = h0v;
+                    *(float4*)&hch[lr][j0 + 4] = h1v;
+                }
+                __syncthreads();
+                {
+                    int lr = tid >> 5;
+                    int i0 = (tid & 31) * 2;
+                    int r  = rbase + lr;
+                    float a0 = 0.f, a1 = 0.f;
+                    #pragma unroll 4
+                    for (int j4 = 0; j4 < NDF; j4 += 4) {
+                        float4 hv = *(const float4*)&hch[lr][j4];
+                        #pragma unroll
+                        for (int s = 0; s < 4; s++) {
+                            float hvs = (s == 0) ? hv.x : (s == 1) ? hv.y
+                                      : (s == 2) ? hv.z : hv.w;
+                            float2 w2v = *(const float2*)(w2 + (j4 + s) * ND + i0);
+                            a0 = fmaf(hvs, w2v.x, a0); a1 = fmaf(hvs, w2v.y, a1);
+                        }
+                    }
+                    float2 bb2 = *(const float2*)(b2 + i0);
+                    xs[r][i0]     += a0 + bb2.x;
+                    xs[r][i0 + 1] += a1 + bb2.y;
+                }
+                __syncthreads();
+            }
+        }
+    }
+    ln_rm(xs, xn, W + OFF_LNFG, W + OFF_LNFB, tid);
+    __syncthreads();
+
+    {
+        const float* lmw = W + OFF_LMW;
+        float wacc = 0.f;
+        for (int rr = 0; rr < 8; rr++) {
+            int r = w * 8 + rr;
+            float lg  = W[OFF_LMB + lane];
+            float lg2 = W[OFF_LMB + 64];
+            #pragma unroll 8
+            for (int i = 0; i < ND; i++) {
+                float xv = xn[r][i];
+                lg  = fmaf(xv, lmw[i * NV + lane], lg);
+                lg2 = fmaf(xv, lmw[i * NV + 64],  lg2);
+            }
+            float M = lg;
+            #pragma unroll
+            for (int off = 32; off; off >>= 1) M = fmaxf(M, __shfl_xor(M, off));
+            M = fmaxf(M, lg2);
+            float ssum = __expf(lg - M);
+            #pragma unroll
+            for (int off = 32; off; off >>= 1) ssum += __shfl_xor(ssum, off);
+            ssum += __expf(lg2 - M);
+            float lse = M + logf(ssum);
+            int row = b * NT + r;
+            int tg  = i64 ? (int)tgt64[row] : tgt32[row];
+            float lt = (tg < 64) ? __shfl(lg, tg) : lg2;
+            wacc += lt - lse;
+            out[row * NV + lane] = lg;
+            if (lane == 0) out[row * NV + 64] = lg2;
+        }
+        if (lane == 0) wsum[w] = wacc;
+        __syncthreads();
+        if (tid == 0) {
+            float t = 0.f;
+            #pragma unroll
+            for (int wv = 0; wv < 16; wv++) t += wsum[wv];
+            atomicAdd(loss_acc, t);
+        }
     }
 }
 
@@ -817,5 +948,7 @@
 
     gpt_fwd<<<NB, 1024, 0, stream>>>(W, pkw, usepk, d_in[19], d_in[20],
                                      (float*)d_out, loss_acc, flags);
+    gpt_fwd_valu<<<NB, 1024, 0, stream>>>(W, usepk, d_in[19], d_in[20],
+                                          (float*)d_out, loss_acc, flags);
     finalize_loss<<<1, 1, 0, stream>>>(loss_acc, (float*)d_out);
 }
```

Result: slower. 4.668 ms (+89.3%).
